# Optimization experiments

Hardware: AMD Instinct MI355X
Metric: run time of the kernel (lower is better)

## Reference

```python
import jax, jax.numpy as jnp
import numpy as np
from jax import lax

D_MODEL = 1024; N_HEADS = 16; D_FF = 4096
D_INNER = 2048; D_STATE = 16; D_CONV = 4; DT_RANK = 64
B = 4; T = 1024; TF = 512
HD = D_MODEL // N_HEADS


def setup_inputs() -> dict:
    key = jax.random.key(0)
    ks = jax.random.split(key, 24)
    r = lambda i, shape, s=0.02: jax.random.normal(ks[i], shape, jnp.float32) * s
    lengths = jnp.array([512, 384, 448, 320])
    styled_mask = jnp.arange(TF)[None, :] < lengths[:, None]  # True = valid
    inp = {
        'x': jax.random.normal(ks[0], (B, T, D_MODEL), jnp.float32),
        'styled_frames': jax.random.normal(ks[1], (B, TF, D_MODEL), jnp.float32),
        'styled_mask': styled_mask,
        'ln1_g': jnp.ones((D_MODEL,)), 'ln1_b': jnp.zeros((D_MODEL,)),
        'ln2_g': jnp.ones((D_MODEL,)), 'ln2_b': jnp.zeros((D_MODEL,)),
        'ln3_g': jnp.ones((D_MODEL,)), 'ln3_b': jnp.zeros((D_MODEL,)),
        'm_in_w': r(2, (D_MODEL, 2 * D_INNER)),
        'm_conv_w': r(3, (D_INNER, D_CONV), 0.1),
        'm_conv_b': jnp.zeros((D_INNER,)),
        'm_xproj_w': r(4, (D_INNER, DT_RANK + 2 * D_STATE)),
        'm_dt_w': r(5, (DT_RANK, D_INNER), 0.1),
        'm_dt_b': jnp.full((D_INNER,), -4.6),  # softplus -> dt ~ 0.01
        'm_A_log': jnp.log(jnp.broadcast_to(jnp.arange(1, D_STATE + 1, dtype=jnp.float32), (D_INNER, D_STATE))),
        'm_D': jnp.ones((D_INNER,)),
        'm_out_w': r(6, (D_INNER, D_MODEL)),
        'attn_in_w': r(7, (3 * D_MODEL, D_MODEL)),
        'attn_in_b': jnp.zeros((3 * D_MODEL,)),
        'attn_out_w': r(8, (D_MODEL, D_MODEL)),
        'attn_out_b': jnp.zeros((D_MODEL,)),
        'ff_w1': r(9, (D_MODEL, D_FF)),
        'ff_b1': jnp.zeros((D_FF,)),
        'ff_w2': r(10, (D_FF, D_MODEL)),
        'ff_b2': jnp.zeros((D_MODEL,)),
    }
    return inp


def _layer_norm(x, g, b):
    m = x.mean(-1, keepdims=True)
    v = ((x - m) ** 2).mean(-1, keepdims=True)
    return (x - m) / jnp.sqrt(v + 1e-5) * g + b


def _mamba(h, m_in_w, m_conv_w, m_conv_b, m_xproj_w, m_dt_w, m_dt_b, m_A_log, m_D, m_out_w):
    xz = h @ m_in_w                                   # (B,T,2*d_inner)
    xm, z = jnp.split(xz, 2, axis=-1)
    # causal depthwise conv1d
    xt = jnp.pad(xm.transpose(0, 2, 1), ((0, 0), (0, 0), (D_CONV - 1, 0)))  # (B,d_inner,T+pad)
    xc = lax.conv_general_dilated(xt, m_conv_w[:, None, :], (1,), 'VALID',
                                  feature_group_count=D_INNER,
                                  dimension_numbers=('NCH', 'OIH', 'NCH'))
    xc = jax.nn.silu(xc + m_conv_b[None, :, None]).transpose(0, 2, 1)       # (B,T,d_inner)
    x_dbl = xc @ m_xproj_w
    dt, Bs, Cs = jnp.split(x_dbl, [DT_RANK, DT_RANK + D_STATE], axis=-1)
    dt = jax.nn.softplus(dt @ m_dt_w + m_dt_b)        # (B,T,d_inner)
    A = -jnp.exp(m_A_log)                             # (d_inner,d_state)

    def step(hs, inp):
        dt_t, B_t, C_t, u_t = inp                     # (B,d_inner),(B,d_state),(B,d_state),(B,d_inner)
        dA = jnp.exp(dt_t[:, :, None] * A)            # (B,d_inner,d_state)
        hs = dA * hs + dt_t[:, :, None] * B_t[:, None, :] * u_t[:, :, None]
        y = jnp.einsum('bds,bs->bd', hs, C_t)
        return hs, y

    h0 = jnp.zeros((xc.shape[0], D_INNER, D_STATE), xc.dtype)
    inputs = (dt.transpose(1, 0, 2), Bs.transpose(1, 0, 2), Cs.transpose(1, 0, 2), xc.transpose(1, 0, 2))
    hT, ys = lax.scan(step, h0, inputs)
    y = ys.transpose(1, 0, 2) + xc * m_D
    y = y * jax.nn.silu(z)
    return y @ m_out_w, hT


def _cross_attn(q_in, kv_in, valid_mask, in_w, in_b, out_w, out_b):
    d = D_MODEL
    q = q_in @ in_w[:d].T + in_b[:d]
    k = kv_in @ in_w[d:2 * d].T + in_b[d:2 * d]
    v = kv_in @ in_w[2 * d:].T + in_b[2 * d:]
    q = q.reshape(q.shape[0], q.shape[1], N_HEADS, HD)
    k = k.reshape(k.shape[0], k.shape[1], N_HEADS, HD)
    v = v.reshape(v.shape[0], v.shape[1], N_HEADS, HD)
    scores = jnp.einsum('bqhd,bkhd->bhqk', q, k) / np.sqrt(HD)
    scores = jnp.where(valid_mask[:, None, None, :], scores, jnp.finfo(scores.dtype).min)
    attn = jax.nn.softmax(scores, axis=-1)
    o = jnp.einsum('bhqk,bkhd->bqhd', attn, v).reshape(q_in.shape)
    return o @ out_w.T + out_b


def reference(x, styled_frames, styled_mask,
              ln1_g, ln1_b, ln2_g, ln2_b, ln3_g, ln3_b,
              m_in_w, m_conv_w, m_conv_b, m_xproj_w, m_dt_w, m_dt_b, m_A_log, m_D, m_out_w,
              attn_in_w, attn_in_b, attn_out_w, attn_out_b,
              ff_w1, ff_b1, ff_w2, ff_b2):
    h = _layer_norm(x, ln1_g, ln1_b)
    h_mamba, new_state = _mamba(h, m_in_w, m_conv_w, m_conv_b, m_xproj_w, m_dt_w, m_dt_b, m_A_log, m_D, m_out_w)
    x = x + h_mamba
    h = _layer_norm(x, ln2_g, ln2_b)
    x = x + _cross_attn(h, styled_frames, styled_mask, attn_in_w, attn_in_b, attn_out_w, attn_out_b)
    h = _layer_norm(x, ln3_g, ln3_b)
    ff = jax.nn.gelu(h @ ff_w1 + ff_b1, approximate=False) @ ff_w2 + ff_b2
    x = x + ff
    return x, new_state
```

## Files before the change

kernel.cpp:

```cpp
#include <hip/hip_runtime.h>
#include <hip/hip_bf16.h>
#include <cstdint>

using bf16 = __hip_bfloat16;

typedef __attribute__((ext_vector_type(8))) short short8;
typedef __attribute__((ext_vector_type(4))) float floatx4;

__device__ __forceinline__ float b2f(bf16 h) { return __bfloat162float(h); }
__device__ __forceinline__ bf16 f2b(float f) { return __float2bfloat16(f); }
__device__ __forceinline__ float uitf(unsigned u) { union { unsigned u; float f; } c; c.u = u; return c.f; }

__device__ __forceinline__ void async16(const bf16* g, bf16* l) {
    __builtin_amdgcn_global_load_lds(
        (const __attribute__((address_space(1))) uint32_t*)(const void*)g,
        (__attribute__((address_space(3))) uint32_t*)(void*)l, 16, 0, 0);
}

__global__ void lens_flag_kernel(const unsigned char* __restrict__ mask,
                                 const unsigned int* __restrict__ ln1g_raw,
                                 int* __restrict__ hdr) {
    __shared__ int cnt[4];
    int tid = threadIdx.x;
    if (tid < 4) cnt[tid] = 0;
    __syncthreads();
    unsigned char b0 = mask[0], b1 = mask[1];
    int width = (b1 == 0) ? 4 : ((b0 == 1) ? 1 : 2);
    if (width == 4) {
        const unsigned int* m = (const unsigned int*)mask;
        for (int i = tid; i < 2048; i += 256) if (m[i] != 0u) atomicAdd(&cnt[i >> 9], 1);
    } else if (width == 2) {
        const unsigned short* m = (const unsigned short*)mask;
        for (int i = tid; i < 2048; i += 256) if (m[i] != 0u) atomicAdd(&cnt[i >> 9], 1);
    } else {
        for (int i = tid; i < 2048; i += 256) if (mask[i] != 0u) atomicAdd(&cnt[i >> 9], 1);
    }
    __syncthreads();
    if (tid < 4) hdr[tid] = cnt[tid];
    if (tid == 4) hdr[4] = (ln1g_raw[0] == 0x3F800000u) ? 1 : 0;
}

__global__ void convert_kernel(const void* __restrict__ src, bf16* __restrict__ dst, int n,
                               const int* __restrict__ flagp) {
    int i = blockIdx.x * 256 + threadIdx.x;
    if (i >= n) return;
    if (*flagp) dst[i] = f2b(((const float*)src)[i]);
    else        dst[i] = ((const bf16*)src)[i];
}

struct SmallSrcs { const void* p[15]; };
__global__ void convert_smalls_kernel(SmallSrcs s, bf16* __restrict__ dst,
                                      const int* __restrict__ flagp) {
    const int ends[16] = {0, 1024, 2048, 3072, 4096, 5120, 6144, 14336, 16384, 18432,
                          51200, 53248, 56320, 57344, 61440, 62464};
    int i = blockIdx.x * 256 + threadIdx.x;
    if (i >= 62464) return;
    int seg = 0;
    #pragma unroll
    for (int k = 1; k < 16; ++k) if (i >= ends[k]) seg = k;
    int local = i - ends[seg];
    const void* sp = s.p[seg];
    if (*flagp) dst[i] = f2b(((const float*)sp)[local]);
    else        dst[i] = ((const bf16*)sp)[local];
}

__global__ void transpose_any(const void* __restrict__ src, bf16* __restrict__ dst,
                              int R, int C, const int* __restrict__ flagp) {
    __shared__ bf16 tile[32][33];
    bool f32 = (*flagp != 0);
    int bx = blockIdx.x * 32, by = blockIdx.y * 32;
    int tx = threadIdx.x;
    for (int i = threadIdx.y; i < 32; i += 8) {
        int y = by + i, x = bx + tx;
        if (y < R && x < C) {
            size_t idx = (size_t)y * C + x;
            tile[i][tx] = f32 ? f2b(((const float*)src)[idx]) : ((const bf16*)src)[idx];
        }
    }
    __syncthreads();
    for (int i = threadIdx.y; i < 32; i += 8) {
        int yo = bx + i, xo = by + tx;
        if (yo < C && xo < R) dst[(size_t)yo * R + xo] = tile[tx][i];
    }
}

__global__ void vtrans_kernel(const bf16* __restrict__ kv, bf16* __restrict__ vt) {
    __shared__ bf16 t[32][33];
    int kc = blockIdx.x * 32, dc = blockIdx.y * 32;
    int bh = blockIdx.z; int b = bh >> 4, h = bh & 15;
    int tx = threadIdx.x;
    for (int i = threadIdx.y; i < 32; i += 8)
        t[i][tx] = kv[(size_t)(b * 512 + kc + i) * 2048 + 1024 + h * 64 + dc + tx];
    __syncthreads();
    for (int i = threadIdx.y; i < 32; i += 8)
        vt[(size_t)(bh * 64 + dc + i) * 512 + kc + tx] = t[tx][i];
}

__global__ __launch_bounds__(256) void ln_kernel(const bf16* __restrict__ x, const bf16* __restrict__ g,
                                                 const bf16* __restrict__ bb, bf16* __restrict__ out) {
    int row = blockIdx.x, tid = threadIdx.x;
    const bf16* xr = x + (size_t)row * 1024;
    float v[4];
    {
        uint2 raw = *(const uint2*)(xr + tid * 4);
        v[0] = uitf(raw.x << 16); v[1] = uitf(raw.x & 0xffff0000u);
        v[2] = uitf(raw.y << 16); v[3] = uitf(raw.y & 0xffff0000u);
    }
    float sum = v[0] + v[1] + v[2] + v[3];
    float sq = v[0]*v[0] + v[1]*v[1] + v[2]*v[2] + v[3]*v[3];
    for (int off = 32; off; off >>= 1) { sum += __shfl_xor(sum, off); sq += __shfl_xor(sq, off); }
    __shared__ float wsm[8];
    int wave = tid >> 6;
    if ((tid & 63) == 0) { wsm[wave * 2] = sum; wsm[wave * 2 + 1] = sq; }
    __syncthreads();
    sum = wsm[0] + wsm[2] + wsm[4] + wsm[6];
    sq  = wsm[1] + wsm[3] + wsm[5] + wsm[7];
    float mean = sum * (1.f / 1024.f);
    float var = sq * (1.f / 1024.f) - mean * mean;
    float rstd = rsqrtf(var + 1e-5f);
    bf16* orow = out + (size_t)row * 1024;
    #pragma unroll
    for (int c = 0; c < 4; ++c) {
        int col = tid * 4 + c;
        orow[col] = f2b((v[c] - mean) * rstd * b2f(g[col]) + b2f(bb[col]));
    }
}

template<int BN>
__global__ __launch_bounds__(256) void gemm_bt(
    const bf16* __restrict__ A, int lda,
    const bf16* __restrict__ Bt, int ldb,
    void* __restrict__ Cp, int ldc, int c_f32,
    int M, int N, int K,
    const bf16* __restrict__ bias,
    const bf16* __restrict__ res, int ldres,
    int act)
{
    constexpr int NJ = BN / 32;
    __shared__ __align__(16) bf16 As[3][128 * 32];
    __shared__ __align__(16) bf16 Bs[3][BN * 32];
    const int tid = threadIdx.x;
    const int lane = tid & 63;
    const int wave = tid >> 6;
    const int wr = (wave >> 1) * 64;
    const int wc = (wave & 1) * (BN / 2);
    const int lrow = lane & 15;
    const int quad = lane >> 4;

    const int gx = gridDim.x;
    const int nwg = gx * gridDim.y;
    const int orig = blockIdx.y * gx + blockIdx.x;
    int wgid = orig;
    if ((nwg & 7) == 0) wgid = (orig & 7) * (nwg >> 3) + (orig >> 3);
    const int n0 = (wgid % gx) * BN;
    const int m0 = (wgid / gx) * 128;

    const int r0 = tid >> 2;
    const int c0 = (((tid & 3) ^ ((r0 >> 1) & 3)) << 3);

    floatx4 acc[4][NJ];
    #pragma unroll
    for (int i = 0; i < 4; ++i)
        #pragma unroll
        for (int j = 0; j < NJ; ++j) acc[i][j] = (floatx4){0.f, 0.f, 0.f, 0.f};

    const int n1 = n0 + r0, n2 = n0 + r0 + 64;
    const bool fullN = (n0 + BN <= N);
    const bool bok1 = n1 < N, bok2 = n2 < N;
    const int4 z4 = {0, 0, 0, 0};

    const bf16* Ag1 = A + (size_t)(m0 + r0) * lda + c0;
    const bf16* Ag2 = A + (size_t)(m0 + r0 + 64) * lda + c0;
    const bf16* Bg1 = Bt + (size_t)n1 * ldb + c0;
    const bf16* Bg2 = Bt + (size_t)n2 * ldb + c0;

    const int chsw = ((quad ^ ((lrow >> 1) & 3)) << 3);
    const int nt = K >> 5;

    if (fullN) {
        auto stage = [&](int buf, int k0) {
            bf16* AsW = &As[buf][tid * 8];
            bf16* BsW = &Bs[buf][tid * 8];
            async16(Ag1 + k0, AsW);
            async16(Ag2 + k0, AsW + 64 * 32);
            async16(Bg1 + k0, BsW);
            if constexpr (BN == 128) async16(Bg2 + k0, BsW + 64 * 32);
        };
        stage(0, 0);
        if (nt > 1) stage(1, 32);
        int cur = 0;
        for (int t = 0; t < nt; ++t) {
            if (t + 1 < nt) {
                if constexpr (BN == 128) asm volatile("s_waitcnt vmcnt(4)" ::: "memory");
                else                     asm volatile("s_waitcnt vmcnt(3)" ::: "memory");
            } else {
                asm volatile("s_waitcnt vmcnt(0)" ::: "memory");
            }
            __builtin_amdgcn_s_barrier();
            __builtin_amdgcn_sched_barrier(0);
            if (t + 2 < nt) {
                int nb = cur + 2; if (nb >= 3) nb -= 3;
                stage(nb, (t + 2) << 5);
            }
            short8 af[4], bfr[NJ];
            #pragma unroll
            for (int i = 0; i < 4; ++i) af[i]  = *(const short8*)&As[cur][(wr + i * 16 + lrow) * 32 + chsw];
            #pragma unroll
            for (int j = 0; j < NJ; ++j) bfr[j] = *(const short8*)&Bs[cur][(wc + j * 16 + lrow) * 32 + chsw];
            #pragma unroll
            for (int i = 0; i < 4; ++i)
                #pragma unroll
                for (int j = 0; j < NJ; ++j)
                    acc[i][j] = __builtin_amdgcn_mfma_f32_16x16x32_bf16(bfr[j], af[i], acc[i][j], 0, 0, 0);
            if (++cur == 3) cur = 0;
        }
    } else {
        bf16* AsW = &As[0][tid * 8];
        bf16* BsW = &Bs[0][tid * 8];
        for (int k0 = 0; k0 < K; k0 += 32) {
            __syncthreads();
            async16(Ag1 + k0, AsW);
            async16(Ag2 + k0, AsW + 64 * 32);
            *(int4*)BsW = bok1 ? *(const int4*)(Bg1 + k0) : z4;
            if constexpr (BN == 128)
                *(int4*)(BsW + 64 * 32) = bok2 ? *(const int4*)(Bg2 + k0) : z4;
            __syncthreads();
            short8 af[4], bfr[NJ];
            #pragma unroll
            for (int i = 0; i < 4; ++i) af[i]  = *(const short8*)&As[0][(wr + i * 16 + lrow) * 32 + chsw];
            #pragma unroll
            for (int j = 0; j < NJ; ++j) bfr[j] = *(const short8*)&Bs[0][(wc + j * 16 + lrow) * 32 + chsw];
            #pragma unroll
            for (int i = 0; i < 4; ++i)
                #pragma unroll
                for (int j = 0; j < NJ; ++j)
                    acc[i][j] = __builtin_amdgcn_mfma_f32_16x16x32_bf16(bfr[j], af[i], acc[i][j], 0, 0, 0);
        }
    }

    #pragma unroll
    for (int i = 0; i < 4; ++i) {
        const int row = m0 + wr + i * 16 + lrow;
        #pragma unroll
        for (int j = 0; j < NJ; ++j) {
            const int col = n0 + wc + j * 16 + quad * 4;
            float v4[4];
            #pragma unroll
            for (int r = 0; r < 4; ++r) {
                float v = acc[i][j][r];
                if (bias) v += b2f(bias[col + r]);
                if (act == 1)      v = 0.5f * v * (1.f + erff(v * 0.70710678118f));
                else if (act == 2) v = (v > 15.f) ? v : log1pf(__expf(v));
                v4[r] = v;
            }
            if (col + 4 <= N) {
                if (res) {
                    uint2 rr = *(const uint2*)(res + (size_t)row * ldres + col);
                    v4[0] += uitf(rr.x << 16); v4[1] += uitf(rr.x & 0xffff0000u);
                    v4[2] += uitf(rr.y << 16); v4[3] += uitf(rr.y & 0xffff0000u);
                }
                if (c_f32) {
                    float4 o = {v4[0], v4[1], v4[2], v4[3]};
                    *(float4*)((float*)Cp + (size_t)row * ldc + col) = o;
                } else {
                    bf16 o[4] = {f2b(v4[0]), f2b(v4[1]), f2b(v4[2]), f2b(v4[3])};
                    *(uint2*)((bf16*)Cp + (size_t)row * ldc + col) = *(uint2*)o;
                }
            } else {
                #pragma unroll
                for (int r = 0; r < 4; ++r) {
                    if (col + r >= N) continue;
                    float v = v4[r];
                    if (res) v += b2f(res[(size_t)row * ldres + col + r]);
                    if (c_f32) ((float*)Cp)[(size_t)row * ldc + col + r] = v;
                    else       ((bf16*)Cp)[(size_t)row * ldc + col + r] = f2b(v);
                }
            }
        }
    }
}

__global__ __launch_bounds__(256) void conv_silu_kernel(const bf16* __restrict__ xz, const bf16* __restrict__ cw,
                                                        const bf16* __restrict__ cb, bf16* __restrict__ xc) {
    int idx = blockIdx.x * 256 + threadIdx.x;
    int d = idx & 2047;
    int row = idx >> 11;
    int t = row & 1023;
    int base = row - t;
    float acc = b2f(cb[d]);
    #pragma unroll
    for (int j = 0; j < 4; ++j) {
        int tt = t - 3 + j;
        if (tt >= 0) acc += b2f(xz[(size_t)(base + tt) * 4096 + d]) * b2f(cw[d * 4 + j]);
    }
    xc[idx] = f2b(acc * (1.f / (1.f + __expf(-acc))));
}

__global__ __launch_bounds__(256) void scan_part1(
    const bf16* __restrict__ dt, const bf16* __restrict__ xc, const bf16* __restrict__ xdbl,
    const bf16* __restrict__ A_log, float* __restrict__ Pb, float* __restrict__ qb)
{
    __shared__ float smB[128][20];
    const int tid = threadIdx.x;
    const int dgrp = blockIdx.x, c = blockIdx.y, b = blockIdx.z;
    const int dl = tid >> 1, sh = tid & 1;
    const int d = (dgrp << 7) + dl;
    const size_t rowbase = (size_t)b * 1024 + (size_t)c * 128;

    {
        int r = tid >> 1, q = tid & 1;
        short8 raw = *(const short8*)(xdbl + (rowbase + r) * 96 + 64 + q * 8);
        #pragma unroll
        for (int j = 0; j < 8; ++j) smB[r][q * 8 + j] = b2f(((const bf16*)&raw)[j]);
    }
    __syncthreads();

    float A2[8], h[8];
    #pragma unroll
    for (int s = 0; s < 8; ++s) {
        A2[s] = -__expf(b2f(A_log[d * 16 + sh * 8 + s])) * 1.44269504f;
        h[s] = 0.f;
    }
    float dtsum = 0.f;
    const bf16* dtp = dt + rowbase * 2048 + d;
    const bf16* up  = xc + rowbase * 2048 + d;
    for (int tc = 0; tc < 128; tc += 8) {
        float dtv[8], uv[8];
        #pragma unroll
        for (int i = 0; i < 8; ++i) {
            dtv[i] = b2f(dtp[(size_t)(tc + i) * 2048]);
            uv[i]  = b2f(up[(size_t)(tc + i) * 2048]);
        }
        #pragma unroll
        for (int i = 0; i < 8; ++i) {
            float dtf = dtv[i];
            dtsum += dtf;
            float w = dtf * uv[i];
            float4 B0 = *(const float4*)&smB[tc + i][sh * 8];
            float4 B1 = *(const float4*)&smB[tc + i][sh * 8 + 4];
            float Bv[8] = {B0.x, B0.y, B0.z, B0.w, B1.x, B1.y, B1.z, B1.w};
            #pragma unroll
            for (int s = 0; s < 8; ++s) {
                float e = __builtin_amdgcn_exp2f(dtf * A2[s]);
                h[s] = fmaf(e, h[s], w * Bv[s]);
            }
        }
    }
    size_t gid = ((size_t)(b * 2048 + d) * 16 + sh * 8) + (size_t)c * 131072;
    float Pv[8];
    #pragma unroll
    for (int s = 0; s < 8; ++s) Pv[s] = __builtin_amdgcn_exp2f(A2[s] * dtsum);
    *(float4*)(Pb + gid)     = *(float4*)&Pv[0];
    *(float4*)(Pb + gid + 4) = *(float4*)&Pv[4];
    *(float4*)(qb + gid)     = *(float4*)&h[0];
    *(float4*)(qb + gid + 4) = *(float4*)&h[4];
}

__global__ __launch_bounds__(256) void scan_stitch(
    const float* __restrict__ Pb, const float* __restrict__ qb,
    float* __restrict__ hs, float* __restrict__ state_out)
{
    int gid = blockIdx.x * 256 + threadIdx.x;
    float h = 0.f;
    #pragma unroll
    for (int c = 0; c < 8; ++c) {
        hs[gid + c * 131072] = h;
        h = Pb[gid + c * 131072] * h + qb[gid + c * 131072];
    }
    state_out[gid] = h;
}

__global__ __launch_bounds__(256) void scan_part3(
    const bf16* __restrict__ dt, const bf16* __restrict__ xc, const bf16* __restrict__ xdbl,
    const bf16* __restrict__ xz, const bf16* __restrict__ A_log, const bf16* __restrict__ Dp,
    const float* __restrict__ hs, bf16* __restrict__ ymul)
{
    __shared__ float smBC[128][36];
    const int tid = threadIdx.x;
    const int dgrp = blockIdx.x, c = blockIdx.y, b = blockIdx.z;
    const int dl = tid >> 1, sh = tid & 1;
    const int d = (dgrp << 7) + dl;
    const size_t rowbase = (size_t)b * 1024 + (size_t)c * 128;

    {
        int r = tid >> 1, q = tid & 1;
        const bf16* src = xdbl + (rowbase + r) * 96 + 64 + q * 16;
        short8 raw0 = *(const short8*)src;
        short8 raw1 = *(const short8*)(src + 8);
        #pragma unroll
        for (int j = 0; j < 8; ++j) {
            smBC[r][q * 16 + j]     = b2f(((const bf16*)&raw0)[j]);
            smBC[r][q * 16 + 8 + j] = b2f(((const bf16*)&raw1)[j]);
        }
    }
    __syncthreads();

    float A2[8], h[8];
    size_t gid = ((size_t)(b * 2048 + d) * 16 + sh * 8) + (size_t)c * 131072;
    {
        float4 h0 = *(const float4*)(hs + gid);
        float4 h1 = *(const float4*)(hs + gid + 4);
        h[0] = h0.x; h[1] = h0.y; h[2] = h0.z; h[3] = h0.w;
        h[4] = h1.x; h[5] = h1.y; h[6] = h1.z; h[7] = h1.w;
    }
    #pragma unroll
    for (int s = 0; s < 8; ++s)
        A2[s] = -__expf(b2f(A_log[d * 16 + sh * 8 + s])) * 1.44269504f;
    const float Dv = b2f(Dp[d]);
    const bf16* dtp = dt + rowbase * 2048 + d;
    const bf16* up  = xc + rowbase * 2048 + d;
    const bf16* zp  = xz + rowbase * 4096 + 2048 + d;
    bf16* yp = ymul + rowbase * 2048 + d;
    for (int tc = 0; tc < 128; tc += 8) {
        float dtv[8], uv[8], zv[8];
        #pragma unroll
        for (int i = 0; i < 8; ++i) {
            dtv[i] = b2f(dtp[(size_t)(tc + i) * 2048]);
            uv[i]  = b2f(up[(size_t)(tc + i) * 2048]);
            zv[i]  = b2f(zp[(size_t)(tc + i) * 4096]);
        }
        #pragma unroll
        for (int i = 0; i < 8; ++i) {
            float dtf = dtv[i], uf = uv[i];
            float w = dtf * uf;
            float4 B0 = *(const float4*)&smBC[tc + i][sh * 8];
            float4 B1 = *(const float4*)&smBC[tc + i][sh * 8 + 4];
            float4 C0 = *(const float4*)&smBC[tc + i][16 + sh * 8];
            float4 C1 = *(const float4*)&smBC[tc + i][16 + sh * 8 + 4];
            float Bv[8] = {B0.x, B0.y, B0.z, B0.w, B1.x, B1.y, B1.z, B1.w};
            float Cv[8] = {C0.x, C0.y, C0.z, C0.w, C1.x, C1.y, C1.z, C1.w};
            float y = 0.f;
            #pragma unroll
            for (int s = 0; s < 8; ++s) {
                float e = __builtin_amdgcn_exp2f(dtf * A2[s]);
                h[s] = fmaf(e, h[s], w * Bv[s]);
                y = fmaf(h[s], Cv[s], y);
            }
            y += __shfl_xor(y, 1);
            float z = zv[i];
            float sig = __builtin_amdgcn_rcpf(1.f + __builtin_amdgcn_exp2f(-1.44269504f * z));
            float o = (y + uf * Dv) * (z * sig);
            if (sh == 0) yp[(size_t)(tc + i) * 2048] = f2b(o);
        }
    }
}

__global__ __launch_bounds__(256) void attn_mfma(
    const bf16* __restrict__ qb, const bf16* __restrict__ kv, const bf16* __restrict__ vt,
    const int* __restrict__ lens, bf16* __restrict__ ob)
{
    const int qt = blockIdx.x, h = blockIdx.y, b = blockIdx.z;
    const int tid = threadIdx.x;
    const int wave = tid >> 6;
    const int lane = tid & 63;
    const int l15 = lane & 15;
    const int quad = lane >> 4;
    const int len = lens[b];

    __shared__ __align__(16) bf16 Ps[32][520];
    __shared__ float red_sh[4][32];

    short8 aq[2][2];
    const bf16* qbase = qb + (size_t)(b * 1024 + qt * 32 + l15) * 1024 + h * 64 + quad * 8;
    #pragma unroll
    for (int mt = 0; mt < 2; ++mt)
        #pragma unroll
        for (int ks = 0; ks < 2; ++ks)
            aq[mt][ks] = *(const short8*)(qbase + (size_t)mt * 16 * 1024 + ks * 32);

    floatx4 accs[2][8];
    #pragma unroll
    for (int mt = 0; mt < 2; ++mt)
        #pragma unroll
        for (int nt = 0; nt < 8; ++nt) accs[mt][nt] = (floatx4){0.f, 0.f, 0.f, 0.f};

    const bf16* kbase = kv + (size_t)(b * 512 + wave * 128 + l15) * 2048 + h * 64 + quad * 8;
    #pragma unroll
    for (int nt = 0; nt < 8; ++nt) {
        short8 bk0 = *(const short8*)(kbase + (size_t)nt * 16 * 2048);
        short8 bk1 = *(const short8*)(kbase + (size_t)nt * 16 * 2048 + 32);
        #pragma unroll
        for (int mt = 0; mt < 2; ++mt) {
            accs[mt][nt] = __builtin_amdgcn_mfma_f32_16x16x32_bf16(aq[mt][0], bk0, accs[mt][nt], 0, 0, 0);
            accs[mt][nt] = __builtin_amdgcn_mfma_f32_16x16x32_bf16(aq[mt][1], bk1, accs[mt][nt], 0, 0, 0);
        }
    }

    float pm[2][4];
    #pragma unroll
    for (int mt = 0; mt < 2; ++mt)
        #pragma unroll
        for (int r = 0; r < 4; ++r) pm[mt][r] = -1e30f;
    #pragma unroll
    for (int mt = 0; mt < 2; ++mt)
        #pragma unroll
        for (int nt = 0; nt < 8; ++nt) {
            int col = wave * 128 + nt * 16 + l15;
            bool ok = col < len;
            #pragma unroll
            for (int r = 0; r < 4; ++r) {
                float s = ok ? accs[mt][nt][r] * 0.125f : -1e30f;
                accs[mt][nt][r] = s;
                pm[mt][r] = fmaxf(pm[mt][r], s);
            }
        }
    #pragma unroll
    for (int off = 1; off < 16; off <<= 1)
        #pragma unroll
        for (int mt = 0; mt < 2; ++mt)
            #pragma unroll
            for (int r = 0; r < 4; ++r) pm[mt][r] = fmaxf(pm[mt][r], __shfl_xor(pm[mt][r], off));
    if (l15 == 0)
        #pragma unroll
        for (int mt = 0; mt < 2; ++mt)
            #pragma unroll
            for (int r = 0; r < 4; ++r) red_sh[wave][mt * 16 + quad * 4 + r] = pm[mt][r];
    __syncthreads();
    float rowmax[2][4];
    #pragma unroll
    for (int mt = 0; mt < 2; ++mt)
        #pragma unroll
        for (int r = 0; r < 4; ++r) {
            int row = mt * 16 + quad * 4 + r;
            rowmax[mt][r] = fmaxf(fmaxf(red_sh[0][row], red_sh[1][row]),
                                  fmaxf(red_sh[2][row], red_sh[3][row]));
        }
    __syncthreads();

    float ps[2][4] = {{0.f, 0.f, 0.f, 0.f}, {0.f, 0.f, 0.f, 0.f}};
    #pragma unroll
    for (int mt = 0; mt < 2; ++mt)
        #pragma unroll
        for (int nt = 0; nt < 8; ++nt)
            #pragma unroll
            for (int r = 0; r < 4; ++r) {
                float p = __expf(accs[mt][nt][r] - rowmax[mt][r]);
                accs[mt][nt][r] = p;
                ps[mt][r] += p;
            }
    #pragma unroll
    for (int off = 1; off < 16; off <<= 1)
        #pragma unroll
        for (int mt = 0; mt < 2; ++mt)
            #pragma unroll
            for (int r = 0; r < 4; ++r) ps[mt][r] += __shfl_xor(ps[mt][r], off);
    if (l15 == 0)
        #pragma unroll
        for (int mt = 0; mt < 2; ++mt)
            #pragma unroll
            for (int r = 0; r < 4; ++r) red_sh[wave][mt * 16 + quad * 4 + r] = ps[mt][r];
    #pragma unroll
    for (int mt = 0; mt < 2; ++mt)
        #pragma unroll
        for (int nt = 0; nt < 8; ++nt)
            #pragma unroll
            for (int r = 0; r < 4; ++r)
                Ps[mt * 16 + quad * 4 + r][wave * 128 + nt * 16 + l15] = f2b(accs[mt][nt][r]);
    __syncthreads();
    float rowsum[2][4];
    #pragma unroll
    for (int mt = 0; mt < 2; ++mt)
        #pragma unroll
        for (int r = 0; r < 4; ++r) {
            int row = mt * 16 + quad * 4 + r;
            rowsum[mt][r] = red_sh[0][row] + red_sh[1][row] + red_sh[2][row] + red_sh[3][row];
        }

    floatx4 acco[2];
    acco[0] = (floatx4){0.f, 0.f, 0.f, 0.f};
    acco[1] = (floatx4){0.f, 0.f, 0.f, 0.f};
    const bf16* vtbase = vt + (size_t)((b * 16 + h) * 64 + wave * 16 + l15) * 512 + quad * 8;
    #pragma unroll
    for (int kc = 0; kc < 16; ++kc) {
        short8 bv = *(const short8*)(vtbase + kc * 32);
        short8 ap0 = *(const short8*)&Ps[l15][kc * 32 + quad * 8];
        short8 ap1 = *(const short8*)&Ps[16 + l15][kc * 32 + quad * 8];
        acco[0] = __builtin_amdgcn_mfma_f32_16x16x32_bf16(ap0, bv, acco[0], 0, 0, 0);
        acco[1] = __builtin_amdgcn_mfma_f32_16x16x32_bf16(ap1, bv, acco[1], 0, 0, 0);
    }

    #pragma unroll
    for (int mt = 0; mt < 2; ++mt)
        #pragma unroll
        for (int r = 0; r < 4; ++r) {
            int row = b * 1024 + qt * 32 + mt * 16 + quad * 4 + r;
            int col = h * 64 + wave * 16 + l15;
            ob[(size_t)row * 1024 + col] = f2b(acco[mt][r] / rowsum[mt][r]);
        }
}

extern "C" void kernel_launch(void* const* d_in, const int* in_sizes, int n_in,
                              void* d_out, int out_size, void* d_ws, size_t ws_size,
                              hipStream_t stream) {
    bf16* W = (bf16*)d_ws;
    int* hdr = (int*)d_ws;
    const int* flagp = hdr + 4;
    const size_t CV_X     = 32;
    const size_t CV_ST    = CV_X    + 4194304;
    const size_t CV_AIW   = CV_ST   + 2097152;
    const size_t CV_AOW   = CV_AIW  + 3145728;
    const size_t CV_SM    = CV_AOW  + 1048576;
    const size_t WT_IN    = CV_SM   + 62464;
    const size_t WT_XPROJ = WT_IN   + 4194304;
    const size_t WT_DT    = WT_XPROJ + 196608;
    const size_t WT_OUT   = WT_DT   + 131072;
    const size_t WT_FF1   = WT_OUT  + 2097152;
    const size_t WT_FF2   = WT_FF1  + 4194304;
    const size_t HB   = WT_FF2 + 4194304;
    const size_t XZ   = HB     + 4194304;
    const size_t XC   = XZ     + 16777216;
    const size_t XDBL = XC     + 8388608;
    const size_t DTB  = XDBL   + 393216;
    const size_t YM   = DTB    + 8388608;
    const size_t X2  = HB;
    const size_t HB2 = DTB;
    const size_t Qb  = XZ;
    const size_t KV  = XZ + 4194304;
    const size_t AO  = XC;
    const size_t VT  = XC + 4194304;
    const size_t X3  = YM;
    const size_t HB3 = DTB;
    const size_t FFH = XZ;
    float* Pb = (float*)(W + HB);
    float* qbuf = Pb + 1048576;
    float* hstart = (float*)(W + WT_IN);
    const size_t S_LN1G = 0, S_LN1B = 1024, S_LN2G = 2048, S_LN2B = 3072, S_LN3G = 4096, S_LN3B = 5120;
    const size_t S_CW = 6144, S_CB = 14336, S_DTB = 16384, S_AL = 18432, S_D = 51200;
    const size_t S_AIB = 53248, S_AOB = 56320, S_FB1 = 57344, S_FB2 = 61440;

    float* out = (float*)d_out;
    float* state_out = out + (size_t)4 * 1024 * 1024;

    lens_flag_kernel<<<1, 256, 0, stream>>>((const unsigned char*)d_in[2],
                                            (const unsigned int*)d_in[3], hdr);
    convert_kernel<<<16384, 256, 0, stream>>>(d_in[0],  W + CV_X,   4194304, flagp);
    convert_kernel<<<8192,  256, 0, stream>>>(d_in[1],  W + CV_ST,  2097152, flagp);
    convert_kernel<<<12288, 256, 0, stream>>>(d_in[18], W + CV_AIW, 3145728, flagp);
    convert_kernel<<<4096,  256, 0, stream>>>(d_in[20], W + CV_AOW, 1048576, flagp);
    SmallSrcs ss;
    ss.p[0] = d_in[3];  ss.p[1] = d_in[4];  ss.p[2] = d_in[5];  ss.p[3] = d_in[6];
    ss.p[4] = d_in[7];  ss.p[5] = d_in[8];  ss.p[6] = d_in[10]; ss.p[7] = d_in[11];
    ss.p[8] = d_in[14]; ss.p[9] = d_in[15]; ss.p[10] = d_in[16]; ss.p[11] = d_in[19];
    ss.p[12] = d_in[21]; ss.p[13] = d_in[23]; ss.p[14] = d_in[25];
    convert_smalls_kernel<<<245, 256, 0, stream>>>(ss, W + CV_SM, flagp);

    dim3 tb(32, 8);
    transpose_any<<<dim3(128, 32), tb, 0, stream>>>(d_in[9],  W + WT_IN,    1024, 4096, flagp);
    transpose_any<<<dim3(3, 64),   tb, 0, stream>>>(d_in[12], W + WT_XPROJ, 2048, 96,   flagp);
    transpose_any<<<dim3(64, 2),   tb, 0, stream>>>(d_in[13], W + WT_DT,    64,   2048, flagp);
    transpose_any<<<dim3(32, 64),  tb, 0, stream>>>(d_in[17], W + WT_OUT,   2048, 1024, flagp);
    transpose_any<<<dim3(128, 32), tb, 0, stream>>>(d_in[22], W + WT_FF1,   1024, 4096, flagp);
    transpose_any<<<dim3(32, 128), tb, 0, stream>>>(d_in[24], W + WT_FF2,   4096, 1024, flagp);

    auto gemm = [&](const bf16* A, int lda, const bf16* Bt, int ldb, void* C, int ldc, int c_f32,
                    int M, int N, int K, const bf16* bias, const bf16* res, int ldres, int act) {
        if ((N & 127) == 0 && N <= 2048) {
            dim3 grid(N / 64, M / 128);
            gemm_bt<64><<<grid, 256, 0, stream>>>(A, lda, Bt, ldb, C, ldc, c_f32, M, N, K, bias, res, ldres, act);
        } else {
            dim3 grid((N + 127) / 128, M / 128);
            gemm_bt<128><<<grid, 256, 0, stream>>>(A, lda, Bt, ldb, C, ldc, c_f32, M, N, K, bias, res, ldres, act);
        }
    };

    ln_kernel<<<4096, 256, 0, stream>>>(W + CV_X, W + CV_SM + S_LN1G, W + CV_SM + S_LN1B, W + HB);
    gemm(W + HB, 1024, W + WT_IN, 1024, W + XZ, 4096, 0, 4096, 4096, 1024, nullptr, nullptr, 0, 0);
    conv_silu_kernel<<<32768, 256, 0, stream>>>(W + XZ, W + CV_SM + S_CW, W + CV_SM + S_CB, W + XC);
    gemm(W + XC, 2048, W + WT_XPROJ, 2048, W + XDBL, 96, 0, 4096, 96, 2048, nullptr, nullptr, 0, 0);
    gemm(W + XDBL, 96, W + WT_DT, 64, W + DTB, 2048, 0, 4096, 2048, 64, W + CV_SM + S_DTB, nullptr, 0, 2);
    scan_part1<<<dim3(16, 8, 4), 256, 0, stream>>>(W + DTB, W + XC, W + XDBL, W + CV_SM + S_AL, Pb, qbuf);
    scan_stitch<<<512, 256, 0, stream>>>(Pb, qbuf, hstart, state_out);
    scan_part3<<<dim3(16, 8, 4), 256, 0, stream>>>(W + DTB, W + XC, W + XDBL, W + XZ,
                                                   W + CV_SM + S_AL, W + CV_SM + S_D, hstart, W + YM);
    gemm(W + YM, 2048, W + WT_OUT, 2048, W + X2, 1024, 0, 4096, 1024, 2048, nullptr, W + CV_X, 1024, 0);

    ln_kernel<<<4096, 256, 0, stream>>>(W + X2, W + CV_SM + S_LN2G, W + CV_SM + S_LN2B, W + HB2);
    gemm(W + HB2, 1024, W + CV_AIW, 1024, W + Qb, 1024, 0, 4096, 1024, 1024, W + CV_SM + S_AIB, nullptr, 0, 0);
    gemm(W + CV_ST, 1024, W + CV_AIW + 1048576, 1024, W + KV, 2048, 0, 2048, 2048, 1024, W + CV_SM + S_AIB + 1024, nullptr, 0, 0);
    vtrans_kernel<<<dim3(16, 2, 64), tb, 0, stream>>>(W + KV, W + VT);
    attn_mfma<<<dim3(32, 16, 4), 256, 0, stream>>>(W + Qb, W + KV, W + VT, hdr, W + AO);
    gemm(W + AO, 1024, W + CV_AOW, 1024, W + X3, 1024, 0, 4096, 1024, 1024, W + CV_SM + S_AOB, W + X2, 1024, 0);

    ln_kernel<<<4096, 256, 0, stream>>>(W + X3, W + CV_SM + S_LN3G, W + CV_SM + S_LN3B, W + HB3);
    gemm(W + HB3, 1024, W + WT_FF1, 1024, W + FFH, 4096, 0, 4096, 4096, 1024, W + CV_SM + S_FB1, nullptr, 0, 1);
    gemm(W + FFH, 4096, W + WT_FF2, 4096, out, 1024, 1, 4096, 1024, 4096, W + CV_SM + S_FB2, W + X3, 1024, 0);
}
```

Before: 899.1 us.

## Add 256x256-tile triple-buffered GEMM kernel for large square-ish GEMMs

Adds a new GEMM kernel with 256x256 output tiles, 512 threads (8 waves each computing 128x64), triple-buffered async global-to-LDS loads with a swizzled layout, and an XCD-aware workgroup remap. The dispatcher routes GEMMs with M and N of at least 4096 to it, which covers the Mamba in-projection and FF1. The aim is more data reuse per tile and better overlap of loads with MFMA work. In exchange each thread holds a large accumulator array, so register pressure rises and occupancy falls, and the grid is smaller (256 blocks for 4096x4096).

```diff
diff --git a/kernel.cpp b/kernel.cpp
--- a/kernel.cpp
+++ b/kernel.cpp
@@ -275,6 +275,116 @@
                     if (c_f32) ((float*)Cp)[(size_t)row * ldc + col + r] = v;
                     else       ((bf16*)Cp)[(size_t)row * ldc + col + r] = f2b(v);
                 }
+            }
+        }
+    }
+}
+
+__global__ __launch_bounds__(512) void gemm_bt_big(
+    const bf16* __restrict__ A, int lda,
+    const bf16* __restrict__ Bt, int ldb,
+    void* __restrict__ Cp, int ldc, int c_f32,
+    int M, int N, int K,
+    const bf16* __restrict__ bias,
+    const bf16* __restrict__ res, int ldres,
+    int act)
+{
+    __shared__ __align__(16) bf16 As[3][256 * 32];
+    __shared__ __align__(16) bf16 Bs[3][256 * 32];
+    const int tid = threadIdx.x;
+    const int lane = tid & 63;
+    const int wave = tid >> 6;
+    const int wm = wave >> 2;
+    const int wn = wave & 3;
+    const int lrow = lane & 15;
+    const int quad = lane >> 4;
+
+    const int gx = gridDim.x;
+    const int nwg = gx * gridDim.y;
+    const int orig = blockIdx.y * gx + blockIdx.x;
+    int wgid = orig;
+    if ((nwg & 7) == 0) wgid = (orig & 7) * (nwg >> 3) + (orig >> 3);
+    const int n0 = (wgid % gx) * 256;
+    const int m0 = (wgid / gx) * 256;
+
+    const int r0 = tid >> 2;
+    const int c0 = (((tid & 3) ^ ((r0 >> 1) & 3)) << 3);
+
+    floatx4 acc[8][4];
+    #pragma unroll
+    for (int i = 0; i < 8; ++i)
+        #pragma unroll
+        for (int j = 0; j < 4; ++j) acc[i][j] = (floatx4){0.f, 0.f, 0.f, 0.f};
+
+    const bf16* Ag1 = A + (size_t)(m0 + r0) * lda + c0;
+    const bf16* Ag2 = A + (size_t)(m0 + r0 + 128) * lda + c0;
+    const bf16* Bg1 = Bt + (size_t)(n0 + r0) * ldb + c0;
+    const bf16* Bg2 = Bt + (size_t)(n0 + r0 + 128) * ldb + c0;
+
+    const int chsw = ((quad ^ ((lrow >> 1) & 3)) << 3);
+    const int nt = K >> 5;
+
+    auto stage = [&](int buf, int k0) {
+        bf16* AsW = &As[buf][tid * 8];
+        bf16* BsW = &Bs[buf][tid * 8];
+        async16(Ag1 + k0, AsW);
+        async16(Ag2 + k0, AsW + 128 * 32);
+        async16(Bg1 + k0, BsW);
+        async16(Bg2 + k0, BsW + 128 * 32);
+    };
+    stage(0, 0);
+    stage(1, 32);
+    int cur = 0;
+    for (int t = 0; t < nt; ++t) {
+        if (t + 1 < nt) asm volatile("s_waitcnt vmcnt(4)" ::: "memory");
+        else            asm volatile("s_waitcnt vmcnt(0)" ::: "memory");
+        __builtin_amdgcn_s_barrier();
+        __builtin_amdgcn_sched_barrier(0);
+        if (t + 2 < nt) {
+            int nb = cur + 2; if (nb >= 3) nb -= 3;
+            stage(nb, (t + 2) << 5);
+        }
+        short8 af[8], bfr[4];
+        #pragma unroll
+        for (int i = 0; i < 8; ++i)
+            af[i] = *(const short8*)&As[cur][(wm * 128 + i * 16 + lrow) * 32 + chsw];
+        #pragma unroll
+        for (int j = 0; j < 4; ++j)
+            bfr[j] = *(const short8*)&Bs[cur][(wn * 64 + j * 16 + lrow) * 32 + chsw];
+        #pragma unroll
+        for (int i = 0; i < 8; ++i)
+            #pragma unroll
+            for (int j = 0; j < 4; ++j)
+                acc[i][j] = __builtin_amdgcn_mfma_f32_16x16x32_bf16(bfr[j], af[i], acc[i][j], 0, 0, 0);
+        if (++cur == 3) cur = 0;
+    }
+
+    #pragma unroll
+    for (int i = 0; i < 8; ++i) {
+        const int row = m0 + wm * 128 + i * 16 + lrow;
+        #pragma unroll
+        for (int j = 0; j < 4; ++j) {
+            const int col = n0 + wn * 64 + j * 16 + quad * 4;
+            float v4[4];
+            #pragma unroll
+            for (int r = 0; r < 4; ++r) {
+                float v = acc[i][j][r];
+                if (bias) v += b2f(bias[col + r]);
+                if (act == 1)      v = 0.5f * v * (1.f + erff(v * 0.70710678118f));
+                else if (act == 2) v = (v > 15.f) ? v : log1pf(__expf(v));
+                v4[r] = v;
+            }
+            if (res) {
+                uint2 rr = *(const uint2*)(res + (size_t)row * ldres + col);
+                v4[0] += uitf(rr.x << 16); v4[1] += uitf(rr.x & 0xffff0000u);
+                v4[2] += uitf(rr.y << 16); v4[3] += uitf(rr.y & 0xffff0000u);
+            }
+            if (c_f32) {
+                float4 o = {v4[0], v4[1], v4[2], v4[3]};
+                *(float4*)((float*)Cp + (size_t)row * ldc + col) = o;
+            } else {
+                bf16 o[4] = {f2b(v4[0]), f2b(v4[1]), f2b(v4[2]), f2b(v4[3])};
+                *(uint2*)((bf16*)Cp + (size_t)row * ldc + col) = *(uint2*)o;
             }
         }
     }
@@ -654,7 +764,10 @@
 
     auto gemm = [&](const bf16* A, int lda, const bf16* Bt, int ldb, void* C, int ldc, int c_f32,
                     int M, int N, int K, const bf16* bias, const bf16* res, int ldres, int act) {
-        if ((N & 127) == 0 && N <= 2048) {
+        if (M >= 4096 && N >= 4096 && (M & 255) == 0 && (N & 255) == 0 && (K & 31) == 0 && K >= 64) {
+            dim3 grid(N / 256, M / 256);
+            gemm_bt_big<<<grid, 512, 0, stream>>>(A, lda, Bt, ldb, C, ldc, c_f32, M, N, K, bias, res, ldres, act);
+        } else if ((N & 127) == 0 && N <= 2048) {
             dim3 grid(N / 64, M / 128);
             gemm_bt<64><<<grid, 256, 0, stream>>>(A, lda, Bt, ldb, C, ldc, c_f32, M, N, K, bias, res, ldres, act);
         } else {
```

After: 929.2 us. +3.3%, slower.
